# Performance work log

Measured on AMD Instinct MI355X. Metric: run time of the kernel, lower is better.

Reference implementation:

```python
import jax, jax.numpy as jnp
import numpy as np

HEAD_DIM = 512 // (8 * 2)  # in_dim // (num_heads * 2) = 32
SQRT2 = np.sqrt(2.0).astype(np.float32)


def dwt1d_haar(x):
    # Haar DWT along last dim: L=(even+odd)/sqrt2, H=(even-odd)/sqrt2
    xe, xo = x[..., 0::2], x[..., 1::2]
    return (xe + xo) / SQRT2, (xe - xo) / SQRT2


def idwt1d_haar(L, H):
    # Inverse: even=(L+H)/sqrt2, odd=(L-H)/sqrt2, interleaved
    even = (L + H) / SQRT2
    odd = (L - H) / SQRT2
    x = jnp.stack([even, odd], axis=-1)  # [..., D/2, 2]
    return x.reshape(*x.shape[:-2], -1)  # [..., D]


def setup_inputs() -> dict:
    key = jax.random.key(0)
    k1, k2, k3, k4 = jax.random.split(key, 4)
    B, S, D = 8, 2048, 512
    queries = jax.random.normal(k1, (B, S, D), dtype=jnp.float32)
    keys = jax.random.normal(k2, (B, S, D), dtype=jnp.float32)
    values = jax.random.normal(k3, (B, S, D), dtype=jnp.float32)
    W_o = jax.random.normal(k4, (D, D), dtype=jnp.float32) * (1.0 / np.sqrt(D))
    b_o = jnp.zeros((D,), dtype=jnp.float32)
    return {"queries": queries, "keys": keys, "values": values, "W_o": W_o, "b_o": b_o}


def reference(queries, keys, values, W_o, b_o):
    scale = 1.0 / jnp.sqrt(jnp.asarray(HEAD_DIM, dtype=queries.dtype))
    q_L, q_H = dwt1d_haar(queries)
    k_L, k_H = dwt1d_haar(keys)
    v_L, v_H = dwt1d_haar(values)
    # [B,S,S] score matrices for each wavelet branch
    attn_L = jax.nn.softmax(jnp.einsum("bqd,bkd->bqk", q_L, k_L) * scale, axis=-1)
    attn_H = jax.nn.softmax(jnp.einsum("bqd,bkd->bqk", q_H, k_H) * scale, axis=-1)
    L_out = jnp.einsum("bqk,bkd->bqd", attn_L, v_L)
    H_out = jnp.einsum("bqk,bkd->bqd", attn_H, v_H)
    output = idwt1d_haar(L_out, H_out)  # [B,S,D]
    return output @ W_o.T + b_o
```

## Files before the change

kernel.cpp:

```cpp
#include <hip/hip_runtime.h>

#define INV_SQRT2 0.70710678118654752f
#define QSCALE    0.17677669529663689f
#define LOG2E     1.44269504088896340f
#define SM_SHIFT  32.0f

typedef __attribute__((ext_vector_type(8))) short bf16x8;
typedef __attribute__((ext_vector_type(4))) float f32x4;
typedef __attribute__((ext_vector_type(16))) float f32x16;

__device__ __forceinline__ unsigned pack2bf(float a, float b) {
  union { float f; unsigned u; } ua, ub; ua.f = a; ub.f = b;
  unsigned ra = ua.u + 0x7FFFu + ((ua.u >> 16) & 1u);
  unsigned rb = ub.u + 0x7FFFu + ((ub.u >> 16) & 1u);
  return __builtin_amdgcn_perm(rb, ra, 0x07060302);
}

__device__ __forceinline__ void async16(const short* g, short* l) {
  typedef __attribute__((address_space(3))) unsigned lds_u32;
  typedef const __attribute__((address_space(1))) unsigned glb_u32;
  __builtin_amdgcn_global_load_lds((glb_u32*)g, (lds_u32*)l, 16, 0, 0);
}

__global__ void dwt_qk(const float* __restrict__ q, const float* __restrict__ k,
                       short* __restrict__ qs, short* __restrict__ ks) {
  int idx = blockIdx.x * 256 + threadIdx.x;
  int j = idx & 31;
  int s = (idx >> 5) & 2047;
  int b = idx >> 16;
  const float4* qp = (const float4*)(q + ((size_t)(b * 2048 + s)) * 512 + j * 16);
  const float4* kp = (const float4*)(k + ((size_t)(b * 2048 + s)) * 512 + j * 16);
  float4 a0 = qp[0], a1 = qp[1], a2 = qp[2], a3 = qp[3];
  float4 c0 = kp[0], c1 = kp[1], c2 = kp[2], c3 = kp[3];
  union { bf16x8 v; unsigned u[4]; } qL, qH, kL, kH;
  const float cs = INV_SQRT2 * QSCALE * LOG2E;
  qL.u[0] = pack2bf((a0.x + a0.y) * cs, (a0.z + a0.w) * cs);
  qL.u[1] = pack2bf((a1.x + a1.y) * cs, (a1.z + a1.w) * cs);
  qL.u[2] = pack2bf((a2.x + a2.y) * cs, (a2.z + a2.w) * cs);
  qL.u[3] = pack2bf((a3.x + a3.y) * cs, (a3.z + a3.w) * cs);
  qH.u[0] = pack2bf((a0.x - a0.y) * cs, (a0.z - a0.w) * cs);
  qH.u[1] = pack2bf((a1.x - a1.y) * cs, (a1.z - a1.w) * cs);
  qH.u[2] = pack2bf((a2.x - a2.y) * cs, (a2.z - a2.w) * cs);
  qH.u[3] = pack2bf((a3.x - a3.y) * cs, (a3.z - a3.w) * cs);
  kL.u[0] = pack2bf((c0.x + c0.y) * INV_SQRT2, (c0.z + c0.w) * INV_SQRT2);
  kL.u[1] = pack2bf((c1.x + c1.y) * INV_SQRT2, (c1.z + c1.w) * INV_SQRT2);
  kL.u[2] = pack2bf((c2.x + c2.y) * INV_SQRT2, (c2.z + c2.w) * INV_SQRT2);
  kL.u[3] = pack2bf((c3.x + c3.y) * INV_SQRT2, (c3.z + c3.w) * INV_SQRT2);
  kH.u[0] = pack2bf((c0.x - c0.y) * INV_SQRT2, (c0.z - c0.w) * INV_SQRT2);
  kH.u[1] = pack2bf((c1.x - c1.y) * INV_SQRT2, (c1.z - c1.w) * INV_SQRT2);
  kH.u[2] = pack2bf((c2.x - c2.y) * INV_SQRT2, (c2.z - c2.w) * INV_SQRT2);
  kH.u[3] = pack2bf((c3.x - c3.y) * INV_SQRT2, (c3.z - c3.w) * INV_SQRT2);
  size_t oL = ((size_t)(b * 2) * 2048 + s) * 256 + j * 8;
  size_t oH = oL + (size_t)2048 * 256;
  *(bf16x8*)(qs + oL) = qL.v;  *(bf16x8*)(qs + oH) = qH.v;
  *(bf16x8*)(ks + oL) = kL.v;  *(bf16x8*)(ks + oH) = kH.v;
}

__global__ void dwt_v(const float* __restrict__ v, short* __restrict__ vt) {
  __shared__ float tL[64][65];
  __shared__ float tH[64][65];
  int t = threadIdx.x;
  int it = blockIdx.x, st = blockIdx.y, b = blockIdx.z;
#pragma unroll
  for (int rep = 0; rep < 8; rep++) {
    int unit = rep * 256 + t;
    int r = unit >> 5, cp = (unit & 31) * 2;
    float4 vv = *(const float4*)(v + ((size_t)(b * 2048 + st * 64 + r)) * 512 + it * 128 + cp * 2);
    tL[r][cp]     = (vv.x + vv.y) * INV_SQRT2;
    tL[r][cp + 1] = (vv.z + vv.w) * INV_SQRT2;
    tH[r][cp]     = (vv.x - vv.y) * INV_SQRT2;
    tH[r][cp + 1] = (vv.z - vv.w) * INV_SQRT2;
  }
  __syncthreads();
#pragma unroll
  for (int rep = 0; rep < 2; rep++) {
    int unit = rep * 256 + t;
    int i = unit >> 3, cc = unit & 7;
    union { bf16x8 v; unsigned u[4]; } pL, pH;
#pragma unroll
    for (int p = 0; p < 4; p++) {
      pL.u[p] = pack2bf(tL[cc * 8 + p * 2][i], tL[cc * 8 + p * 2 + 1][i]);
      pH.u[p] = pack2bf(tH[cc * 8 + p * 2][i], tH[cc * 8 + p * 2 + 1][i]);
    }
    size_t o = ((size_t)(b * 2) * 256 + it * 64 + i) * 2048 + st * 64 + cc * 8;
    *(bf16x8*)(vt + o) = pL.v;
    *(bf16x8*)(vt + o + (size_t)256 * 2048) = pH.v;
  }
}

__launch_bounds__(256, 2)
__global__ void flash_attn(const short* __restrict__ qs, const short* __restrict__ ks,
                           const short* __restrict__ vt, short* __restrict__ os) {
  __shared__ short lds[36864];
  short* klds = lds;
  short* vlds = lds + 16384;
  short* plds = lds + 32768;

  int tid = threadIdx.x;
  int w = tid >> 6, L = tid & 63;
  int lq = L & 31, hi = L >> 5;
  int qt = w & 1, ct = w >> 1;
  int bb = blockIdx.x, qb = blockIdx.y;

  bf16x8 qf[16];
  const short* qptr = qs + (((size_t)bb * 2048) + qb * 64 + qt * 32 + lq) * 256 + hi * 8;
#pragma unroll
  for (int ksI = 0; ksI < 16; ksI++)
    qf[ksI] = *(const bf16x8*)(qptr + ksI * 16);

  f32x16 oacc[4];
#pragma unroll
  for (int mt = 0; mt < 4; mt++)
#pragma unroll
    for (int i = 0; i < 16; i++) oacc[mt][i] = 0.f;
  float l_i = 0.f;

  const short* kbase = ks + ((size_t)bb * 2048) * 256;
  const short* vbase = vt + ((size_t)bb * 256) * 2048;

  int koff[8], voff[8];
#pragma unroll
  for (int rep = 0; rep < 8; rep++) {
    int o = w * 8 + rep;
    int r = 2 * o + (L >> 5);
    int c = (L & 31) ^ (r & 7);
    koff[rep] = r * 256 + c * 8;
    int n = 8 * o + (L >> 3);
    int cv = (L & 7) ^ (n & 7);
    voff[rep] = n * 2048 + cv * 8;
  }

  int krow = ct * 32 + lq, ksw = krow & 7;
  int qrow = qt * 32 + lq, qsw = qrow & 7;

#pragma unroll
  for (int rep = 0; rep < 8; rep++)
    async16(kbase + koff[rep], klds + (w * 8 + rep) * 512);
  __syncthreads();

  for (int kt = 0; kt < 32; kt++) {
#pragma unroll
    for (int rep = 0; rep < 8; rep++)
      async16(vbase + (size_t)kt * 64 + voff[rep], vlds + (w * 8 + rep) * 512);

    f32x16 s0, s1;
#pragma unroll
    for (int i = 0; i < 16; i++) { s0[i] = 0.f; s1[i] = 0.f; }
#pragma unroll
    for (int ksI = 0; ksI < 16; ksI += 2) {
      bf16x8 kb0 = *(const bf16x8*)(klds + krow * 256 + (((ksI << 1) | hi) ^ ksw) * 8);
      bf16x8 kb1 = *(const bf16x8*)(klds + krow * 256 + ((((ksI + 1) << 1) | hi) ^ ksw) * 8);
      s0 = __builtin_amdgcn_mfma_f32_32x32x16_bf16(kb0, qf[ksI], s0, 0, 0, 0);
      s1 = __builtin_amdgcn_mfma_f32_32x32x16_bf16(kb1, qf[ksI + 1], s1, 0, 0, 0);
    }

    float sacc[16];
    float rs = 0.f;
#pragma unroll
    for (int i = 0; i < 16; i++) {
      float p = exp2f((s0[i] + s1[i]) - SM_SHIFT);
      sacc[i] = p;
      rs += p;
    }
    l_i += rs;

#pragma unroll
    for (int g = 0; g < 4; g++) {
      uint2 d;
      d.x = pack2bf(sacc[4 * g], sacc[4 * g + 1]);
      d.y = pack2bf(sacc[4 * g + 2], sacc[4 * g + 3]);
      *(uint2*)(plds + qrow * 64 + ((4 * ct + g) ^ qsw) * 8 + hi * 4) = d;
    }
    __syncthreads();

    if (kt < 31) {
#pragma unroll
      for (int rep = 0; rep < 8; rep++)
        async16(kbase + (size_t)(kt + 1) * 16384 + koff[rep], klds + (w * 8 + rep) * 512);
    }

    bf16x8 pb[4];
#pragma unroll
    for (int ks4 = 0; ks4 < 4; ks4++)
      pb[ks4] = *(const bf16x8*)(plds + qrow * 64 + (((ks4 << 1) | hi) ^ qsw) * 8);
#pragma unroll
    for (int mt = 0; mt < 4; mt++) {
      int vrow = ct * 128 + mt * 32 + lq, vsw = vrow & 7;
#pragma unroll
      for (int ks4 = 0; ks4 < 4; ks4++) {
        bf16x8 vb = *(const bf16x8*)(vlds + vrow * 64 + (((ks4 << 1) | hi) ^ vsw) * 8);
        oacc[mt] = __builtin_amdgcn_mfma_f32_32x32x16_bf16(vb, pb[ks4], oacc[mt], 0, 0, 0);
      }
    }
    __syncthreads();
  }

  float lt = l_i + __shfl_xor(l_i, 32, 64);
  float* lbuf = (float*)plds;
  if (hi == 0) lbuf[(ct * 2 + qt) * 32 + lq] = lt;
  __syncthreads();
  float inv = 1.f / (lt + lbuf[((ct ^ 1) * 2 + qt) * 32 + lq]);

#pragma unroll
  for (int mt = 0; mt < 4; mt++)
#pragma unroll
    for (int g = 0; g < 4; g++) {
      uint2 d;
      d.x = pack2bf(oacc[mt][4 * g] * inv, oacc[mt][4 * g + 1] * inv);
      d.y = pack2bf(oacc[mt][4 * g + 2] * inv, oacc[mt][4 * g + 3] * inv);
      *(uint2*)(lds + qrow * 264 + ct * 128 + mt * 32 + 8 * g + 4 * hi) = d;
    }
  __syncthreads();
  short* obase = os + (((size_t)bb * 2048) + qb * 64) * 256;
#pragma unroll
  for (int rep = 0; rep < 8; rep++) {
    int cid = rep * 256 + tid;
    int row = cid >> 5, c = cid & 31;
    *(bf16x8*)(obase + row * 256 + c * 8) = *(const bf16x8*)(lds + row * 264 + c * 8);
  }
}

__global__ void w2k(const float* __restrict__ W, short* __restrict__ w2) {
  int idx = blockIdx.x * 256 + threadIdx.x;
  int j = idx >> 6, i4 = (idx & 63) * 4;
  const float4* src = (const float4*)(W + (size_t)j * 512 + 2 * i4);
  float4 f0 = src[0], f1 = src[1];
  uint2 dl, dh;
  dl.x = pack2bf((f0.x + f0.y) * INV_SQRT2, (f0.z + f0.w) * INV_SQRT2);
  dl.y = pack2bf((f1.x + f1.y) * INV_SQRT2, (f1.z + f1.w) * INV_SQRT2);
  dh.x = pack2bf((f0.x - f0.y) * INV_SQRT2, (f0.z - f0.w) * INV_SQRT2);
  dh.y = pack2bf((f1.x - f1.y) * INV_SQRT2, (f1.z - f1.w) * INV_SQRT2);
  *(uint2*)(w2 + (size_t)j * 512 + i4) = dl;
  *(uint2*)(w2 + (size_t)j * 512 + 256 + i4) = dh;
}

__launch_bounds__(256, 2)
__global__ void out_gemm(const short* __restrict__ os, const short* __restrict__ w2,
                         const float* __restrict__ bo, float* __restrict__ out) {
  __shared__ short alds[128 * 72];
  __shared__ short blds[128 * 72];
  int tid = threadIdx.x;
  int w = tid >> 6, L = tid & 63, lo = L & 15, hi = L >> 4;
  int wr = w >> 1, wc = w & 1;
  int br = blockIdx.x, bc = blockIdx.y;

  f32x4 acc[4][4];
#pragma unroll
  for (int mt = 0; mt < 4; mt++)
#pragma unroll
    for (int nt = 0; nt < 4; nt++)
      acc[mt][nt] = (f32x4){0.f, 0.f, 0.f, 0.f};

  for (int kt = 0; kt < 8; kt++) {
    __syncthreads();
#pragma unroll
    for (int rep = 0; rep < 4; rep++) {
      int cid = rep * 256 + tid;
      int mrow = cid >> 3, c = cid & 7;
      int gk = kt * 64 + c * 8;
      int half = gk >> 8, i = gk & 255;
      int gr = br * 128 + mrow;
      int b = gr >> 11, s = gr & 2047;
      *(bf16x8*)(alds + mrow * 72 + c * 8) =
          *(const bf16x8*)(os + ((size_t)((b * 2 + half) * 2048 + s)) * 256 + i);
    }
#pragma unroll
    for (int rep = 0; rep < 4; rep++) {
      int cid = rep * 256 + tid;
      int nrow = cid >> 3, c = cid & 7;
      *(bf16x8*)(blds + nrow * 72 + c * 8) =
          *(const bf16x8*)(w2 + (size_t)(bc * 128 + nrow) * 512 + kt * 64 + c * 8);
    }
    __syncthreads();
    bf16x8 af[4], bfr[4];
#pragma unroll
    for (int kc = 0; kc < 2; kc++) {
#pragma unroll
      for (int mt = 0; mt < 4; mt++)
        af[mt] = *(const bf16x8*)(alds + (wr * 64 + mt * 16 + lo) * 72 + kc * 32 + hi * 8);
#pragma unroll
      for (int nt = 0; nt < 4; nt++)
        bfr[nt] = *(const bf16x8*)(blds + (wc * 64 + nt * 16 + lo) * 72 + kc * 32 + hi * 8);
#pragma unroll
      for (int mt = 0; mt < 4; mt++)
#pragma unroll
        for (int nt = 0; nt < 4; nt++)
          acc[mt][nt] = __builtin_amdgcn_mfma_f32_16x16x32_bf16(af[mt], bfr[nt], acc[mt][nt], 0, 0, 0);
    }
  }

#pragma unroll
  for (int nt = 0; nt < 4; nt++) {
    int cc = bc * 128 + wc * 64 + nt * 16 + lo;
    float bias = bo[cc];
#pragma unroll
    for (int mt = 0; mt < 4; mt++) {
      int rrbase = br * 128 + wr * 64 + mt * 16 + hi * 4;
#pragma unroll
      for (int r = 0; r < 4; r++)
        out[(size_t)(rrbase + r) * 512 + cc] = acc[mt][nt][r] + bias;
    }
  }
}

extern "C" void kernel_launch(void* const* d_in, const int* in_sizes, int n_in,
                              void* d_out, int out_size, void* d_ws, size_t ws_size,
                              hipStream_t stream) {
  const float* q  = (const float*)d_in[0];
  const float* k  = (const float*)d_in[1];
  const float* v  = (const float*)d_in[2];
  const float* W  = (const float*)d_in[3];
  const float* bo = (const float*)d_in[4];
  short* ws  = (short*)d_ws;
  short* qs  = ws;
  short* ksb = ws + (size_t)8  * 1024 * 1024;
  short* vtp = ws + (size_t)16 * 1024 * 1024;
  short* osb = ws + (size_t)24 * 1024 * 1024;
  short* w2  = ws + (size_t)32 * 1024 * 1024;

  dwt_qk<<<2048, 256, 0, stream>>>(q, k, qs, ksb);
  dwt_v<<<dim3(4, 32, 8), 256, 0, stream>>>(v, vtp);
  w2k<<<128, 256, 0, stream>>>(W, w2);
  flash_attn<<<dim3(16, 32), 256, 0, stream>>>(qs, ksb, vtp, osb);
  out_gemm<<<dim3(128, 4), 256, 0, stream>>>(osb, w2, bo, (float*)d_out);
}
```

Before: 262.1 us.

## Warp-specialize flash attention into QK/softmax and PV groups; merge preprocessing kernels

Flash attention now runs 512 threads per block, split into two groups of four waves. One group computes QK scores and the exponentials and writes P to LDS. The other group loads V and accumulates PV one tile behind, with the two groups synchronizing through block barriers, so score and PV work can overlap. The three preprocessing kernels (Q/K DWT, V DWT and transpose, W transform) are merged into one launch branched on block index to cut launch overhead. The risks are higher register pressure and more barriers per iteration, and a single P buffer between the groups limits how much overlap is possible.

```diff
diff --git a/kernel.cpp b/kernel.cpp
--- a/kernel.cpp
+++ b/kernel.cpp
@@ -22,73 +22,89 @@
   __builtin_amdgcn_global_load_lds((glb_u32*)g, (lds_u32*)l, 16, 0, 0);
 }
 
-__global__ void dwt_qk(const float* __restrict__ q, const float* __restrict__ k,
-                       short* __restrict__ qs, short* __restrict__ ks) {
-  int idx = blockIdx.x * 256 + threadIdx.x;
-  int j = idx & 31;
-  int s = (idx >> 5) & 2047;
-  int b = idx >> 16;
-  const float4* qp = (const float4*)(q + ((size_t)(b * 2048 + s)) * 512 + j * 16);
-  const float4* kp = (const float4*)(k + ((size_t)(b * 2048 + s)) * 512 + j * 16);
-  float4 a0 = qp[0], a1 = qp[1], a2 = qp[2], a3 = qp[3];
-  float4 c0 = kp[0], c1 = kp[1], c2 = kp[2], c3 = kp[3];
-  union { bf16x8 v; unsigned u[4]; } qL, qH, kL, kH;
-  const float cs = INV_SQRT2 * QSCALE * LOG2E;
-  qL.u[0] = pack2bf((a0.x + a0.y) * cs, (a0.z + a0.w) * cs);
-  qL.u[1] = pack2bf((a1.x + a1.y) * cs, (a1.z + a1.w) * cs);
-  qL.u[2] = pack2bf((a2.x + a2.y) * cs, (a2.z + a2.w) * cs);
-  qL.u[3] = pack2bf((a3.x + a3.y) * cs, (a3.z + a3.w) * cs);
-  qH.u[0] = pack2bf((a0.x - a0.y) * cs, (a0.z - a0.w) * cs);
-  qH.u[1] = pack2bf((a1.x - a1.y) * cs, (a1.z - a1.w) * cs);
-  qH.u[2] = pack2bf((a2.x - a2.y) * cs, (a2.z - a2.w) * cs);
-  qH.u[3] = pack2bf((a3.x - a3.y) * cs, (a3.z - a3.w) * cs);
-  kL.u[0] = pack2bf((c0.x + c0.y) * INV_SQRT2, (c0.z + c0.w) * INV_SQRT2);
-  kL.u[1] = pack2bf((c1.x + c1.y) * INV_SQRT2, (c1.z + c1.w) * INV_SQRT2);
-  kL.u[2] = pack2bf((c2.x + c2.y) * INV_SQRT2, (c2.z + c2.w) * INV_SQRT2);
-  kL.u[3] = pack2bf((c3.x + c3.y) * INV_SQRT2, (c3.z + c3.w) * INV_SQRT2);
-  kH.u[0] = pack2bf((c0.x - c0.y) * INV_SQRT2, (c0.z - c0.w) * INV_SQRT2);
-  kH.u[1] = pack2bf((c1.x - c1.y) * INV_SQRT2, (c1.z - c1.w) * INV_SQRT2);
-  kH.u[2] = pack2bf((c2.x - c2.y) * INV_SQRT2, (c2.z - c2.w) * INV_SQRT2);
-  kH.u[3] = pack2bf((c3.x - c3.y) * INV_SQRT2, (c3.z - c3.w) * INV_SQRT2);
-  size_t oL = ((size_t)(b * 2) * 2048 + s) * 256 + j * 8;
-  size_t oH = oL + (size_t)2048 * 256;
-  *(bf16x8*)(qs + oL) = qL.v;  *(bf16x8*)(qs + oH) = qH.v;
-  *(bf16x8*)(ks + oL) = kL.v;  *(bf16x8*)(ks + oH) = kH.v;
-}
-
-__global__ void dwt_v(const float* __restrict__ v, short* __restrict__ vt) {
+__global__ void dwt_all(const float* __restrict__ q, const float* __restrict__ k,
+                        const float* __restrict__ v, const float* __restrict__ W,
+                        short* __restrict__ qs, short* __restrict__ ks,
+                        short* __restrict__ vt, short* __restrict__ w2) {
   __shared__ float tL[64][65];
   __shared__ float tH[64][65];
+  int bi = blockIdx.x;
   int t = threadIdx.x;
-  int it = blockIdx.x, st = blockIdx.y, b = blockIdx.z;
-#pragma unroll
-  for (int rep = 0; rep < 8; rep++) {
-    int unit = rep * 256 + t;
-    int r = unit >> 5, cp = (unit & 31) * 2;
-    float4 vv = *(const float4*)(v + ((size_t)(b * 2048 + st * 64 + r)) * 512 + it * 128 + cp * 2);
-    tL[r][cp]     = (vv.x + vv.y) * INV_SQRT2;
-    tL[r][cp + 1] = (vv.z + vv.w) * INV_SQRT2;
-    tH[r][cp]     = (vv.x - vv.y) * INV_SQRT2;
-    tH[r][cp + 1] = (vv.z - vv.w) * INV_SQRT2;
-  }
-  __syncthreads();
-#pragma unroll
-  for (int rep = 0; rep < 2; rep++) {
-    int unit = rep * 256 + t;
-    int i = unit >> 3, cc = unit & 7;
-    union { bf16x8 v; unsigned u[4]; } pL, pH;
-#pragma unroll
-    for (int p = 0; p < 4; p++) {
-      pL.u[p] = pack2bf(tL[cc * 8 + p * 2][i], tL[cc * 8 + p * 2 + 1][i]);
-      pH.u[p] = pack2bf(tH[cc * 8 + p * 2][i], tH[cc * 8 + p * 2 + 1][i]);
-    }
-    size_t o = ((size_t)(b * 2) * 256 + it * 64 + i) * 2048 + st * 64 + cc * 8;
-    *(bf16x8*)(vt + o) = pL.v;
-    *(bf16x8*)(vt + o + (size_t)256 * 2048) = pH.v;
-  }
-}
-
-__launch_bounds__(256, 2)
+  if (bi < 2048) {
+    int idx = bi * 256 + t;
+    int j = idx & 31;
+    int s = (idx >> 5) & 2047;
+    int b = idx >> 16;
+    const float4* qp = (const float4*)(q + ((size_t)(b * 2048 + s)) * 512 + j * 16);
+    const float4* kp = (const float4*)(k + ((size_t)(b * 2048 + s)) * 512 + j * 16);
+    float4 a0 = qp[0], a1 = qp[1], a2 = qp[2], a3 = qp[3];
+    float4 c0 = kp[0], c1 = kp[1], c2 = kp[2], c3 = kp[3];
+    union { bf16x8 v; unsigned u[4]; } qL, qH, kL, kH;
+    const float cs = INV_SQRT2 * QSCALE * LOG2E;
+    qL.u[0] = pack2bf((a0.x + a0.y) * cs, (a0.z + a0.w) * cs);
+    qL.u[1] = pack2bf((a1.x + a1.y) * cs, (a1.z + a1.w) * cs);
+    qL.u[2] = pack2bf((a2.x + a2.y) * cs, (a2.z + a2.w) * cs);
+    qL.u[3] = pack2bf((a3.x + a3.y) * cs, (a3.z + a3.w) * cs);
+    qH.u[0] = pack2bf((a0.x - a0.y) * cs, (a0.z - a0.w) * cs);
+    qH.u[1] = pack2bf((a1.x - a1.y) * cs, (a1.z - a1.w) * cs);
+    qH.u[2] = pack2bf((a2.x - a2.y) * cs, (a2.z - a2.w) * cs);
+    qH.u[3] = pack2bf((a3.x - a3.y) * cs, (a3.z - a3.w) * cs);
+    kL.u[0] = pack2bf((c0.x + c0.y) * INV_SQRT2, (c0.z + c0.w) * INV_SQRT2);
+    kL.u[1] = pack2bf((c1.x + c1.y) * INV_SQRT2, (c1.z + c1.w) * INV_SQRT2);
+    kL.u[2] = pack2bf((c2.x + c2.y) * INV_SQRT2, (c2.z + c2.w) * INV_SQRT2);
+    kL.u[3] = pack2bf((c3.x + c3.y) * INV_SQRT2, (c3.z + c3.w) * INV_SQRT2);
+    kH.u[0] = pack2bf((c0.x - c0.y) * INV_SQRT2, (c0.z - c0.w) * INV_SQRT2);
+    kH.u[1] = pack2bf((c1.x - c1.y) * INV_SQRT2, (c1.z - c1.w) * INV_SQRT2);
+    kH.u[2] = pack2bf((c2.x - c2.y) * INV_SQRT2, (c2.z - c2.w) * INV_SQRT2);
+    kH.u[3] = pack2bf((c3.x - c3.y) * INV_SQRT2, (c3.z - c3.w) * INV_SQRT2);
+    size_t oL = ((size_t)(b * 2) * 2048 + s) * 256 + j * 8;
+    size_t oH = oL + (size_t)2048 * 256;
+    *(bf16x8*)(qs + oL) = qL.v;  *(bf16x8*)(qs + oH) = qH.v;
+    *(bf16x8*)(ks + oL) = kL.v;  *(bf16x8*)(ks + oH) = kH.v;
+  } else if (bi < 3072) {
+    int bi2 = bi - 2048;
+    int it = bi2 & 3, st = (bi2 >> 2) & 31, b = bi2 >> 7;
+#pragma unroll
+    for (int rep = 0; rep < 8; rep++) {
+      int unit = rep * 256 + t;
+      int r = unit >> 5, cp = (unit & 31) * 2;
+      float4 vv = *(const float4*)(v + ((size_t)(b * 2048 + st * 64 + r)) * 512 + it * 128 + cp * 2);
+      tL[r][cp]     = (vv.x + vv.y) * INV_SQRT2;
+      tL[r][cp + 1] = (vv.z + vv.w) * INV_SQRT2;
+      tH[r][cp]     = (vv.x - vv.y) * INV_SQRT2;
+      tH[r][cp + 1] = (vv.z - vv.w) * INV_SQRT2;
+    }
+    __syncthreads();
+#pragma unroll
+    for (int rep = 0; rep < 2; rep++) {
+      int unit = rep * 256 + t;
+      int i = unit >> 3, cc = unit & 7;
+      union { bf16x8 v; unsigned u[4]; } pL, pH;
+#pragma unroll
+      for (int p = 0; p < 4; p++) {
+        pL.u[p] = pack2bf(tL[cc * 8 + p * 2][i], tL[cc * 8 + p * 2 + 1][i]);
+        pH.u[p] = pack2bf(tH[cc * 8 + p * 2][i], tH[cc * 8 + p * 2 + 1][i]);
+      }
+      size_t o = ((size_t)(b * 2) * 256 + it * 64 + i) * 2048 + st * 64 + cc * 8;
+      *(bf16x8*)(vt + o) = pL.v;
+      *(bf16x8*)(vt + o + (size_t)256 * 2048) = pH.v;
+    }
+  } else {
+    int idx = (bi - 3072) * 256 + t;
+    int j = idx >> 6, i4 = (idx & 63) * 4;
+    const float4* src = (const float4*)(W + (size_t)j * 512 + 2 * i4);
+    float4 f0 = src[0], f1 = src[1];
+    uint2 dl, dh;
+    dl.x = pack2bf((f0.x + f0.y) * INV_SQRT2, (f0.z + f0.w) * INV_SQRT2);
+    dl.y = pack2bf((f1.x + f1.y) * INV_SQRT2, (f1.z + f1.w) * INV_SQRT2);
+    dh.x = pack2bf((f0.x - f0.y) * INV_SQRT2, (f0.z - f0.w) * INV_SQRT2);
+    dh.y = pack2bf((f1.x - f1.y) * INV_SQRT2, (f1.z - f1.w) * INV_SQRT2);
+    *(uint2*)(w2 + (size_t)j * 512 + i4) = dl;
+    *(uint2*)(w2 + (size_t)j * 512 + 256 + i4) = dh;
+  }
+}
+
+__launch_bounds__(512, 4)
 __global__ void flash_attn(const short* __restrict__ qs, const short* __restrict__ ks,
                            const short* __restrict__ vt, short* __restrict__ os) {
   __shared__ short lds[36864];
@@ -99,139 +115,150 @@
   int tid = threadIdx.x;
   int w = tid >> 6, L = tid & 63;
   int lq = L & 31, hi = L >> 5;
-  int qt = w & 1, ct = w >> 1;
   int bb = blockIdx.x, qb = blockIdx.y;
-
-  bf16x8 qf[16];
-  const short* qptr = qs + (((size_t)bb * 2048) + qb * 64 + qt * 32 + lq) * 256 + hi * 8;
-#pragma unroll
-  for (int ksI = 0; ksI < 16; ksI++)
-    qf[ksI] = *(const bf16x8*)(qptr + ksI * 16);
-
-  f32x16 oacc[4];
-#pragma unroll
-  for (int mt = 0; mt < 4; mt++)
-#pragma unroll
-    for (int i = 0; i < 16; i++) oacc[mt][i] = 0.f;
-  float l_i = 0.f;
 
   const short* kbase = ks + ((size_t)bb * 2048) * 256;
   const short* vbase = vt + ((size_t)bb * 256) * 2048;
-
-  int koff[8], voff[8];
-#pragma unroll
-  for (int rep = 0; rep < 8; rep++) {
-    int o = w * 8 + rep;
-    int r = 2 * o + (L >> 5);
-    int c = (L & 31) ^ (r & 7);
-    koff[rep] = r * 256 + c * 8;
-    int n = 8 * o + (L >> 3);
-    int cv = (L & 7) ^ (n & 7);
-    voff[rep] = n * 2048 + cv * 8;
-  }
-
-  int krow = ct * 32 + lq, ksw = krow & 7;
-  int qrow = qt * 32 + lq, qsw = qrow & 7;
-
-#pragma unroll
-  for (int rep = 0; rep < 8; rep++)
-    async16(kbase + koff[rep], klds + (w * 8 + rep) * 512);
-  __syncthreads();
-
-  for (int kt = 0; kt < 32; kt++) {
+  short* obase = os + (((size_t)bb * 2048) + qb * 64) * 256;
+
+  if (w < 4) {
+    int ct = w >> 1, qt = w & 1;
+    int krow = ct * 32 + lq, ksw = krow & 7;
+    int qrow = qt * 32 + lq, qsw = qrow & 7;
+
+    int koff[8];
+#pragma unroll
+    for (int rep = 0; rep < 8; rep++) {
+      int o = w * 8 + rep;
+      int r = 2 * o + (L >> 5);
+      int c = (L & 31) ^ (r & 7);
+      koff[rep] = r * 256 + c * 8;
+    }
 #pragma unroll
     for (int rep = 0; rep < 8; rep++)
-      async16(vbase + (size_t)kt * 64 + voff[rep], vlds + (w * 8 + rep) * 512);
-
-    f32x16 s0, s1;
-#pragma unroll
-    for (int i = 0; i < 16; i++) { s0[i] = 0.f; s1[i] = 0.f; }
-#pragma unroll
-    for (int ksI = 0; ksI < 16; ksI += 2) {
-      bf16x8 kb0 = *(const bf16x8*)(klds + krow * 256 + (((ksI << 1) | hi) ^ ksw) * 8);
-      bf16x8 kb1 = *(const bf16x8*)(klds + krow * 256 + ((((ksI + 1) << 1) | hi) ^ ksw) * 8);
-      s0 = __builtin_amdgcn_mfma_f32_32x32x16_bf16(kb0, qf[ksI], s0, 0, 0, 0);
-      s1 = __builtin_amdgcn_mfma_f32_32x32x16_bf16(kb1, qf[ksI + 1], s1, 0, 0, 0);
-    }
-
-    float sacc[16];
-    float rs = 0.f;
-#pragma unroll
-    for (int i = 0; i < 16; i++) {
-      float p = exp2f((s0[i] + s1[i]) - SM_SHIFT);
-      sacc[i] = p;
-      rs += p;
-    }
-    l_i += rs;
-
-#pragma unroll
-    for (int g = 0; g < 4; g++) {
-      uint2 d;
-      d.x = pack2bf(sacc[4 * g], sacc[4 * g + 1]);
-      d.y = pack2bf(sacc[4 * g + 2], sacc[4 * g + 3]);
-      *(uint2*)(plds + qrow * 64 + ((4 * ct + g) ^ qsw) * 8 + hi * 4) = d;
-    }
-    __syncthreads();
-
-    if (kt < 31) {
-#pragma unroll
-      for (int rep = 0; rep < 8; rep++)
-        async16(kbase + (size_t)(kt + 1) * 16384 + koff[rep], klds + (w * 8 + rep) * 512);
-    }
-
-    bf16x8 pb[4];
-#pragma unroll
-    for (int ks4 = 0; ks4 < 4; ks4++)
-      pb[ks4] = *(const bf16x8*)(plds + qrow * 64 + (((ks4 << 1) | hi) ^ qsw) * 8);
-#pragma unroll
-    for (int mt = 0; mt < 4; mt++) {
-      int vrow = ct * 128 + mt * 32 + lq, vsw = vrow & 7;
-#pragma unroll
-      for (int ks4 = 0; ks4 < 4; ks4++) {
-        bf16x8 vb = *(const bf16x8*)(vlds + vrow * 64 + (((ks4 << 1) | hi) ^ vsw) * 8);
-        oacc[mt] = __builtin_amdgcn_mfma_f32_32x32x16_bf16(vb, pb[ks4], oacc[mt], 0, 0, 0);
-      }
-    }
-    __syncthreads();
-  }
-
-  float lt = l_i + __shfl_xor(l_i, 32, 64);
-  float* lbuf = (float*)plds;
-  if (hi == 0) lbuf[(ct * 2 + qt) * 32 + lq] = lt;
-  __syncthreads();
-  float inv = 1.f / (lt + lbuf[((ct ^ 1) * 2 + qt) * 32 + lq]);
-
-#pragma unroll
-  for (int mt = 0; mt < 4; mt++)
-#pragma unroll
-    for (int g = 0; g < 4; g++) {
-      uint2 d;
-      d.x = pack2bf(oacc[mt][4 * g] * inv, oacc[mt][4 * g + 1] * inv);
-      d.y = pack2bf(oacc[mt][4 * g + 2] * inv, oacc[mt][4 * g + 3] * inv);
-      *(uint2*)(lds + qrow * 264 + ct * 128 + mt * 32 + 8 * g + 4 * hi) = d;
-    }
-  __syncthreads();
-  short* obase = os + (((size_t)bb * 2048) + qb * 64) * 256;
-#pragma unroll
-  for (int rep = 0; rep < 8; rep++) {
-    int cid = rep * 256 + tid;
+      async16(kbase + koff[rep], klds + (w * 8 + rep) * 512);
+
+    bf16x8 qf[16];
+    const short* qptr = qs + (((size_t)bb * 2048) + qb * 64 + qrow) * 256 + hi * 8;
+#pragma unroll
+    for (int ksI = 0; ksI < 16; ksI++)
+      qf[ksI] = *(const bf16x8*)(qptr + ksI * 16);
+
+    float l_i = 0.f;
+    __syncthreads();
+
+    for (int it = 0; it <= 32; ++it) {
+      f32x16 s0, s1;
+      if (it < 32) {
+#pragma unroll
+        for (int i = 0; i < 16; i++) { s0[i] = 0.f; s1[i] = 0.f; }
+#pragma unroll
+        for (int ksI = 0; ksI < 16; ksI += 2) {
+          bf16x8 kb0 = *(const bf16x8*)(klds + krow * 256 + (((ksI << 1) | hi) ^ ksw) * 8);
+          bf16x8 kb1 = *(const bf16x8*)(klds + krow * 256 + ((((ksI + 1) << 1) | hi) ^ ksw) * 8);
+          s0 = __builtin_amdgcn_mfma_f32_32x32x16_bf16(kb0, qf[ksI], s0, 0, 0, 0);
+          s1 = __builtin_amdgcn_mfma_f32_32x32x16_bf16(kb1, qf[ksI + 1], s1, 0, 0, 0);
+        }
+      }
+      __syncthreads();
+      if (it < 32) {
+        if (it < 31) {
+#pragma unroll
+          for (int rep = 0; rep < 8; rep++)
+            async16(kbase + (size_t)(it + 1) * 16384 + koff[rep], klds + (w * 8 + rep) * 512);
+        }
+        float rs = 0.f;
+#pragma unroll
+        for (int g = 0; g < 4; g++) {
+          float p0 = exp2f(s0[4 * g]     + s1[4 * g]     - SM_SHIFT);
+          float p1 = exp2f(s0[4 * g + 1] + s1[4 * g + 1] - SM_SHIFT);
+          float p2 = exp2f(s0[4 * g + 2] + s1[4 * g + 2] - SM_SHIFT);
+          float p3 = exp2f(s0[4 * g + 3] + s1[4 * g + 3] - SM_SHIFT);
+          rs += (p0 + p1) + (p2 + p3);
+          uint2 d; d.x = pack2bf(p0, p1); d.y = pack2bf(p2, p3);
+          *(uint2*)(plds + qrow * 64 + ((4 * ct + g) ^ qsw) * 8 + hi * 4) = d;
+        }
+        l_i += rs;
+      }
+      __syncthreads();
+    }
+    float lt = l_i + __shfl_xor(l_i, 32, 64);
+    if (hi == 0) ((float*)plds)[(ct * 2 + qt) * 32 + lq] = lt;
+    __syncthreads();
+    __syncthreads();
+  } else {
+    int cw = w - 4;
+    int voff[8];
+#pragma unroll
+    for (int rep = 0; rep < 8; rep++) {
+      int o = cw * 8 + rep;
+      int n = 8 * o + (L >> 3);
+      int cv = (L & 7) ^ (n & 7);
+      voff[rep] = n * 2048 + cv * 8;
+    }
+#pragma unroll
+    for (int rep = 0; rep < 8; rep++)
+      async16(vbase + voff[rep], vlds + (cw * 8 + rep) * 512);
+
+    f32x16 oacc[4];
+#pragma unroll
+    for (int m = 0; m < 4; m++)
+#pragma unroll
+      for (int i = 0; i < 16; i++) oacc[m][i] = 0.f;
+
+    int vr0 = cw * 64 + lq, vr1 = cw * 64 + 32 + lq;
+    int sw = lq & 7;
+    __syncthreads();
+
+    for (int it = 0; it <= 32; ++it) {
+      if (it > 0) {
+#pragma unroll
+        for (int ks4 = 0; ks4 < 4; ks4++) {
+          int ch = (((ks4 << 1) | hi) ^ sw) * 8;
+          bf16x8 pb0 = *(const bf16x8*)(plds + lq * 64 + ch);
+          bf16x8 pb1 = *(const bf16x8*)(plds + (32 + lq) * 64 + ch);
+          bf16x8 vb0 = *(const bf16x8*)(vlds + vr0 * 64 + ch);
+          bf16x8 vb1 = *(const bf16x8*)(vlds + vr1 * 64 + ch);
+          oacc[0] = __builtin_amdgcn_mfma_f32_32x32x16_bf16(vb0, pb0, oacc[0], 0, 0, 0);
+          oacc[1] = __builtin_amdgcn_mfma_f32_32x32x16_bf16(vb0, pb1, oacc[1], 0, 0, 0);
+          oacc[2] = __builtin_amdgcn_mfma_f32_32x32x16_bf16(vb1, pb0, oacc[2], 0, 0, 0);
+          oacc[3] = __builtin_amdgcn_mfma_f32_32x32x16_bf16(vb1, pb1, oacc[3], 0, 0, 0);
+        }
+      }
+      __syncthreads();
+      if (it >= 1 && it < 32) {
+#pragma unroll
+        for (int rep = 0; rep < 8; rep++)
+          async16(vbase + (size_t)it * 64 + voff[rep], vlds + (cw * 8 + rep) * 512);
+      }
+      __syncthreads();
+    }
+    __syncthreads();
+    const float* lbuf = (const float*)plds;
+    float inv0 = 1.f / (lbuf[lq] + lbuf[64 + lq]);
+    float inv1 = 1.f / (lbuf[32 + lq] + lbuf[96 + lq]);
+#pragma unroll
+    for (int ot = 0; ot < 4; ot++) {
+      float inv = (ot & 1) ? inv1 : inv0;
+      int qg = (ot & 1) * 32 + lq;
+      int colb = cw * 64 + (ot >> 1) * 32 + 4 * hi;
+#pragma unroll
+      for (int g = 0; g < 4; g++) {
+        uint2 d;
+        d.x = pack2bf(oacc[ot][4 * g] * inv, oacc[ot][4 * g + 1] * inv);
+        d.y = pack2bf(oacc[ot][4 * g + 2] * inv, oacc[ot][4 * g + 3] * inv);
+        *(uint2*)(lds + qg * 264 + colb + 8 * g) = d;
+      }
+    }
+    __syncthreads();
+  }
+
+#pragma unroll
+  for (int rep = 0; rep < 4; rep++) {
+    int cid = rep * 512 + tid;
     int row = cid >> 5, c = cid & 31;
     *(bf16x8*)(obase + row * 256 + c * 8) = *(const bf16x8*)(lds + row * 264 + c * 8);
   }
-}
-
-__global__ void w2k(const float* __restrict__ W, short* __restrict__ w2) {
-  int idx = blockIdx.x * 256 + threadIdx.x;
-  int j = idx >> 6, i4 = (idx & 63) * 4;
-  const float4* src = (const float4*)(W + (size_t)j * 512 + 2 * i4);
-  float4 f0 = src[0], f1 = src[1];
-  uint2 dl, dh;
-  dl.x = pack2bf((f0.x + f0.y) * INV_SQRT2, (f0.z + f0.w) * INV_SQRT2);
-  dl.y = pack2bf((f1.x + f1.y) * INV_SQRT2, (f1.z + f1.w) * INV_SQRT2);
-  dh.x = pack2bf((f0.x - f0.y) * INV_SQRT2, (f0.z - f0.w) * INV_SQRT2);
-  dh.y = pack2bf((f1.x - f1.y) * INV_SQRT2, (f1.z - f1.w) * INV_SQRT2);
-  *(uint2*)(w2 + (size_t)j * 512 + i4) = dl;
-  *(uint2*)(w2 + (size_t)j * 512 + 256 + i4) = dh;
 }
 
 __launch_bounds__(256, 2)
@@ -318,9 +345,7 @@
   short* osb = ws + (size_t)24 * 1024 * 1024;
   short* w2  = ws + (size_t)32 * 1024 * 1024;
 
-  dwt_qk<<<2048, 256, 0, stream>>>(q, k, qs, ksb);
-  dwt_v<<<dim3(4, 32, 8), 256, 0, stream>>>(v, vtp);
-  w2k<<<128, 256, 0, stream>>>(W, w2);
-  flash_attn<<<dim3(16, 32), 256, 0, stream>>>(qs, ksb, vtp, osb);
+  dwt_all<<<3200, 256, 0, stream>>>(q, k, v, W, qs, ksb, vtp, w2);
+  flash_attn<<<dim3(16, 32), 512, 0, stream>>>(qs, ksb, vtp, osb);
   out_gemm<<<dim3(128, 4), 256, 0, stream>>>(osb, w2, bo, (float*)d_out);
 }
```

Result: slower. 269.0 us (+2.7%).
